# Optimization experiments

Hardware: AMD Instinct MI355X
Metric: run time of the kernel (lower is better)

## Reference

```python
import jax, jax.numpy as jnp
import numpy as np

STD = 0.5
B = 1048576
DIM = 8  # arch == 2
_LOG_STD = -0.6931471805599453       # log(0.5)
_HALF_LOG_2PI = 0.9189385332046727   # 0.5*log(2*pi)


def _mlp(x, w1, b1, w2, b2):
    # Sequential(Linear, ReLU, Linear)
    return jnp.maximum(x @ w1 + b1, 0.0) @ w2 + b2


def _bce_sum(logits, targets):
    # BCEWithLogitsLoss(reduction='sum'), numerically stable
    return jnp.sum(jnp.maximum(logits, 0.0) - logits * targets
                   + jnp.log1p(jnp.exp(-jnp.abs(logits))))


def _normal_logprob_sum(mu, y):
    # D.Normal(mu, STD).log_prob(y).sum()
    return jnp.sum(-0.5 * ((y - mu) / STD) ** 2 - _LOG_STD - _HALF_LOG_2PI)


def setup_inputs() -> dict:
    key = jax.random.key(0)
    keys = iter(jax.random.split(key, 64))

    def nrm(shape, s=1.0):
        return s * jax.random.normal(next(keys), shape, dtype=jnp.float32)

    inp = {
        'y1': nrm((B, 1)),
        'y2': nrm((B, 1)),
        'n1': jax.random.uniform(next(keys), (B, 2), dtype=jnp.float32),
        'n2': jax.random.uniform(next(keys), (B, 2), dtype=jnp.float32),
        'n3': jax.random.uniform(next(keys), (B, 2), dtype=jnp.float32),
        'n4': jax.random.uniform(next(keys), (B, 2), dtype=jnp.float32),
    }
    # (name, d_in, d_out) for every 2-layer MLP in infnet/gennet
    mlp_specs = [('inf0', 2, 2), ('inf1', 3, 2), ('inf2', 1, 2), ('inf3', 2, 2),
                 ('g1', 2, 2), ('g2', 2, 1), ('g3', 1, 2), ('g4', 2, 2), ('g5', 2, 1)]
    for name, din, dout in mlp_specs:
        inp[name + '_w1'] = nrm((din, DIM), 0.5)
        inp[name + '_b1'] = nrm((DIM,), 0.1)
        inp[name + '_w2'] = nrm((DIM, dout), 0.5)
        inp[name + '_b2'] = nrm((dout,), 0.1)
    inp['g0_w'] = nrm((1, 2), 0.5)  # gennet[0]: Linear(1, z, bias=False)
    return inp


def reference(y1, y2, n1, n2, n3, n4,
              inf0_w1, inf0_b1, inf0_w2, inf0_b2,
              inf1_w1, inf1_b1, inf1_w2, inf1_b2,
              inf2_w1, inf2_b1, inf2_w2, inf2_b2,
              inf3_w1, inf3_b1, inf3_w2, inf3_b2,
              g1_w1, g1_b1, g1_w2, g1_b2,
              g2_w1, g2_b1, g2_w2, g2_b2,
              g3_w1, g3_b1, g3_w2, g3_b2,
              g4_w1, g4_b1, g4_w2, g4_b2,
              g5_w1, g5_b1, g5_w2, g5_b2,
              g0_w):
    b = y1.shape[0]
    # ---- infer(): recognition pass with hard Bernoulli samples ----
    pz1 = jax.nn.sigmoid(_mlp(jnp.concatenate([y1, y2], axis=1),
                              inf0_w1, inf0_b1, inf0_w2, inf0_b2))
    z1 = (pz1 > n1).astype(jnp.float32)
    pz2 = jax.nn.sigmoid(_mlp(jnp.concatenate([y2, z1], axis=1),
                              inf1_w1, inf1_b1, inf1_w2, inf1_b2))
    z2 = (pz2 > n2).astype(jnp.float32)
    pz3 = jax.nn.sigmoid(_mlp(y2, inf2_w1, inf2_b1, inf2_w2, inf2_b2))
    z3 = (pz3 > n3).astype(jnp.float32)
    pz4 = jax.nn.sigmoid(_mlp(z3, inf3_w1, inf3_b1, inf3_w2, inf3_b2))
    z4 = (pz4 > n4).astype(jnp.float32)
    # ---- generate_wake(): generative logits conditioned on inferred latents ----
    l4 = jnp.ones((b, 1), jnp.float32) @ g0_w          # [B, 2]
    l3 = _mlp(z4, g1_w1, g1_b1, g1_w2, g1_b2)          # [B, 2]
    muy2 = _mlp(z3, g2_w1, g2_b1, g2_w2, g2_b2)        # [B, 1]
    l2 = _mlp(y2, g3_w1, g3_b1, g3_w2, g3_b2)          # [B, 2]
    l1 = _mlp(z2, g4_w1, g4_b1, g4_w2, g4_b2)          # [B, 2]
    muy1 = _mlp(z1, g5_w1, g5_b1, g5_w2, g5_b2)        # [B, 1]
    # ---- wake losses ----
    bf = jnp.float32(b)
    loss_z = (_bce_sum(l1, z1) + _bce_sum(l2, z2)
              + _bce_sum(l3, z3) + _bce_sum(l4, z4)) / bf
    loss_y = (-_normal_logprob_sum(muy1, y1)
              - _normal_logprob_sum(muy2, y2)) / bf
    return (loss_z + loss_y, loss_z, loss_y)
```

## Files before the change

### kernel.cpp

```cpp
#include <hip/hip_runtime.h>
#include <math.h>

#define NBLK 4096
#define NT 256
#define TBL_OFF (NBLK * 8)

typedef float f32x2 __attribute__((ext_vector_type(2)));

__device__ __forceinline__ f32x2 relu2(f32x2 v) {
    f32x2 z = {0.0f, 0.0f};
    return __builtin_elementwise_max(v, z);
}
__device__ __forceinline__ float zsel(float s, float n) {
    float e = __expf(-s);
    return (1.0f - n > n * e) ? 1.0f : 0.0f;
}
__device__ __forceinline__ float sp_f(float l) {
    return fmaxf(l, 0.0f) + __logf(1.0f + __expf(-fabsf(l)));
}

__global__ __launch_bounds__(64) void make_tables(
    const float* __restrict__ i3w1, const float* __restrict__ i3b1,
    const float* __restrict__ i3w2, const float* __restrict__ i3b2,
    const float* __restrict__ g1w1, const float* __restrict__ g1b1,
    const float* __restrict__ g1w2, const float* __restrict__ g1b2,
    const float* __restrict__ g2w1, const float* __restrict__ g2b1,
    const float* __restrict__ g2w2, const float* __restrict__ g2b2,
    const float* __restrict__ g4w1, const float* __restrict__ g4b1,
    const float* __restrict__ g4w2, const float* __restrict__ g4b2,
    const float* __restrict__ g5w1, const float* __restrict__ g5b1,
    const float* __restrict__ g5w2, const float* __restrict__ g5b2,
    float* __restrict__ tbl)
{
    __shared__ float lds_eval[5][4][2];
    const int tid = threadIdx.x;
    if (tid < 20) {
        const int m = tid >> 2, c = tid & 3;
        const float z0 = (float)(c & 1), z1f = (float)(c >> 1);
        const float *w1, *bb1, *w2, *bb2; int dout;
        switch (m) {
            case 0:  w1 = i3w1; bb1 = i3b1; w2 = i3w2; bb2 = i3b2; dout = 2; break;
            case 1:  w1 = g1w1; bb1 = g1b1; w2 = g1w2; bb2 = g1b2; dout = 2; break;
            case 2:  w1 = g2w1; bb1 = g2b1; w2 = g2w2; bb2 = g2b2; dout = 1; break;
            case 3:  w1 = g4w1; bb1 = g4b1; w2 = g4w2; bb2 = g4b2; dout = 2; break;
            default: w1 = g5w1; bb1 = g5b1; w2 = g5w2; bb2 = g5b2; dout = 1; break;
        }
        float o0 = bb2[0];
        float o1 = (dout == 2) ? bb2[1] : 0.0f;
        #pragma unroll
        for (int j = 0; j < 8; ++j) {
            float h = fmaxf(bb1[j] + z0 * w1[j] + z1f * w1[8 + j], 0.0f);
            o0 += h * w2[j * dout];
            if (dout == 2) o1 += h * w2[j * 2 + 1];
        }
        lds_eval[m][c][0] = o0;
        lds_eval[m][c][1] = o1;
    }
    __syncthreads();
    if (tid < 12) {
        const int pair = tid >> 1, elem = tid & 1;
        int m, k, tf;
        switch (tid) {
            case 0:  m = 0; k = 0; tf = 1; break;
            case 1:  m = 0; k = 1; tf = 1; break;
            case 2:  m = 1; k = 0; tf = 0; break;
            case 3:  m = 1; k = 1; tf = 0; break;
            case 4:  m = 1; k = 0; tf = 2; break;
            case 5:  m = 1; k = 1; tf = 2; break;
            case 6:  m = 3; k = 0; tf = 0; break;
            case 7:  m = 3; k = 1; tf = 0; break;
            case 8:  m = 3; k = 0; tf = 2; break;
            case 9:  m = 3; k = 1; tf = 2; break;
            case 10: m = 2; k = 0; tf = 0; break;
            default: m = 4; k = 0; tf = 0; break;
        }
        float f[4];
        #pragma unroll
        for (int c = 0; c < 4; ++c) {
            float x = lds_eval[m][c][k];
            if (tf == 1)      x = 1.0f / (1.0f + expf(-x));
            else if (tf == 2) x = fmaxf(x, 0.0f) + log1pf(expf(-fabsf(x)));
            f[c] = x;
        }
        tbl[(pair * 4 + 0) * 2 + elem] = f[0];
        tbl[(pair * 4 + 1) * 2 + elem] = f[1] - f[0];
        tbl[(pair * 4 + 2) * 2 + elem] = f[2] - f[0];
        tbl[(pair * 4 + 3) * 2 + elem] = f[3] - f[1] - f[2] + f[0];
    }
}

#define WPAIR(ptr, idx) (f32x2{(ptr)[idx], (ptr)[(idx) + 1]})

__global__ __launch_bounds__(NT, 6) void wake_main(
    const float* __restrict__ y1, const float* __restrict__ y2,
    const float* __restrict__ n1, const float* __restrict__ n2,
    const float* __restrict__ n3, const float* __restrict__ n4,
    const float* __restrict__ i0w1, const float* __restrict__ i0b1,
    const float* __restrict__ i0w2, const float* __restrict__ i0b2,
    const float* __restrict__ i1w1, const float* __restrict__ i1b1,
    const float* __restrict__ i1w2, const float* __restrict__ i1b2,
    const float* __restrict__ i2w1, const float* __restrict__ i2b1,
    const float* __restrict__ i2w2, const float* __restrict__ i2b2,
    const float* __restrict__ g3w1, const float* __restrict__ g3b1,
    const float* __restrict__ g3w2, const float* __restrict__ g3b2,
    const float* __restrict__ g0w,
    const float* __restrict__ tbl,
    float2* __restrict__ partials)
{
    const int tid = threadIdx.x;
    const int g = blockIdx.x * NT + tid;

    const float Y1 = y1[g];
    const float Y2 = y2[g];
    const float2 N1 = reinterpret_cast<const float2*>(n1)[g];
    const float2 N2 = reinterpret_cast<const float2*>(n2)[g];
    const float2 N3 = reinterpret_cast<const float2*>(n3)[g];
    const float2 N4 = reinterpret_cast<const float2*>(n4)[g];

    f32x2 acc0 = WPAIR(i0b2, 0);
    #pragma unroll
    for (int jp = 0; jp < 4; ++jp) {
        const int j = 2 * jp;
        f32x2 h = relu2(WPAIR(i0b1, j) + Y1 * WPAIR(i0w1, j) + Y2 * WPAIR(i0w1, 8 + j));
        acc0 += h.x * WPAIR(i0w2, 2 * j) + h.y * WPAIR(i0w2, 2 * j + 2);
    }
    const float z10 = zsel(acc0.x, N1.x);
    const float z11 = zsel(acc0.y, N1.y);

    f32x2 acc1 = WPAIR(i1b2, 0);
    #pragma unroll
    for (int jp = 0; jp < 4; ++jp) {
        const int j = 2 * jp;
        f32x2 h = relu2(WPAIR(i1b1, j) + Y2 * WPAIR(i1w1, j)
                        + z10 * WPAIR(i1w1, 8 + j) + z11 * WPAIR(i1w1, 16 + j));
        acc1 += h.x * WPAIR(i1w2, 2 * j) + h.y * WPAIR(i1w2, 2 * j + 2);
    }
    const float z20 = zsel(acc1.x, N2.x);
    const float z21 = zsel(acc1.y, N2.y);

    f32x2 acc2 = WPAIR(i2b2, 0);
    #pragma unroll
    for (int jp = 0; jp < 4; ++jp) {
        const int j = 2 * jp;
        f32x2 h = relu2(WPAIR(i2b1, j) + Y2 * WPAIR(i2w1, j));
        acc2 += h.x * WPAIR(i2w2, 2 * j) + h.y * WPAIR(i2w2, 2 * j + 2);
    }
    const float z30 = zsel(acc2.x, N3.x);
    const float z31 = zsel(acc2.y, N3.y);

    const float p3 = z30 * z31;
    const f32x2 sg = WPAIR(tbl, 0) + z30 * WPAIR(tbl, 2) + z31 * WPAIR(tbl, 4) + p3 * WPAIR(tbl, 6);
    const float z40 = (sg.x > N4.x) ? 1.0f : 0.0f;
    const float z41 = (sg.y > N4.y) ? 1.0f : 0.0f;
    const float p4 = z40 * z41;

    f32x2 l2 = WPAIR(g3b2, 0);
    #pragma unroll
    for (int jp = 0; jp < 4; ++jp) {
        const int j = 2 * jp;
        f32x2 h = relu2(WPAIR(g3b1, j) + Y2 * WPAIR(g3w1, j));
        l2 += h.x * WPAIR(g3w2, 2 * j) + h.y * WPAIR(g3w2, 2 * j + 2);
    }

    const f32x2 l3  = WPAIR(tbl, 8)  + z40 * WPAIR(tbl, 10) + z41 * WPAIR(tbl, 12) + p4 * WPAIR(tbl, 14);
    const f32x2 SP3 = WPAIR(tbl, 16) + z40 * WPAIR(tbl, 18) + z41 * WPAIR(tbl, 20) + p4 * WPAIR(tbl, 22);
    const float p2 = z20 * z21;
    const f32x2 l1  = WPAIR(tbl, 24) + z20 * WPAIR(tbl, 26) + z21 * WPAIR(tbl, 28) + p2 * WPAIR(tbl, 30);
    const f32x2 SP1 = WPAIR(tbl, 32) + z20 * WPAIR(tbl, 34) + z21 * WPAIR(tbl, 36) + p2 * WPAIR(tbl, 38);
    const float p1 = z10 * z11;
    const f32x2 zA = {z30, z10}, zB = {z31, z11}, zP = {p3, p1};
    const f32x2 mu = WPAIR(tbl, 40) + zA * WPAIR(tbl, 42) + zB * WPAIR(tbl, 44) + zP * WPAIR(tbl, 46);
    const float L40 = g0w[0], L41 = g0w[1];

    const f32x2 z1v = {z10, z11}, z2v = {z20, z21}, z3v = {z30, z31};
    f32x2 sp2 = {sp_f(l2.x), sp_f(l2.y)};
    f32x2 bsum = (SP1 - l1 * z1v) + (SP3 - l3 * z3v) + (sp2 - l2 * z2v);
    float lz = bsum.x + bsum.y - (L40 * z40 + L41 * z41);
    const f32x2 d = {Y2 - mu.x, Y1 - mu.y};
    const f32x2 dd = d * d;
    float ly = dd.x + dd.y;

    #pragma unroll
    for (int off = 32; off > 0; off >>= 1) {
        lz += __shfl_down(lz, off);
        ly += __shfl_down(ly, off);
    }
    __shared__ float2 wsum[NT / 64];
    const int lane = tid & 63, wid = tid >> 6;
    if (lane == 0) wsum[wid] = make_float2(lz, ly);
    __syncthreads();
    if (tid == 0) {
        float a = 0.0f, b = 0.0f;
        #pragma unroll
        for (int w = 0; w < NT / 64; ++w) { a += wsum[w].x; b += wsum[w].y; }
        partials[blockIdx.x] = make_float2(a, b);
    }
}

__global__ __launch_bounds__(256) void wake_reduce(
    const float2* __restrict__ partials, const float* __restrict__ g0w,
    float* __restrict__ out)
{
    const int tid = threadIdx.x;
    float lz = 0.0f, ly = 0.0f;
    #pragma unroll
    for (int i = 0; i < NBLK / 256; ++i) {
        float2 p = partials[tid + i * 256];
        lz += p.x; ly += p.y;
    }
    #pragma unroll
    for (int off = 32; off > 0; off >>= 1) {
        lz += __shfl_down(lz, off);
        ly += __shfl_down(ly, off);
    }
    __shared__ float2 wsum[4];
    const int lane = tid & 63, wid = tid >> 6;
    if (lane == 0) wsum[wid] = make_float2(lz, ly);
    __syncthreads();
    if (tid == 0) {
        float a = 0.0f, b = 0.0f;
        #pragma unroll
        for (int w = 0; w < 4; ++w) { a += wsum[w].x; b += wsum[w].y; }
        const float l40 = g0w[0], l41 = g0w[1];
        const float c4 = fmaxf(l40, 0.0f) + log1pf(expf(-fabsf(l40)))
                       + fmaxf(l41, 0.0f) + log1pf(expf(-fabsf(l41)));
        const float inv = 1.0f / 1048576.0f;
        const float loss_z = a * inv + c4;
        const float loss_y = 2.0f * b * inv + 0.4515827052894548f;
        out[0] = loss_z + loss_y;
        out[1] = loss_z;
        out[2] = loss_y;
    }
}

extern "C" void kernel_launch(void* const* d_in, const int* in_sizes, int n_in,
                              void* d_out, int out_size, void* d_ws, size_t ws_size,
                              hipStream_t stream) {
    const float* p[43];
    for (int i = 0; i < 43; ++i) p[i] = (const float*)d_in[i];
    float2* partials = (float2*)d_ws;
    float* tbl = (float*)((char*)d_ws + TBL_OFF);

    make_tables<<<1, 64, 0, stream>>>(
        p[18], p[19], p[20], p[21],
        p[22], p[23], p[24], p[25],
        p[26], p[27], p[28], p[29],
        p[34], p[35], p[36], p[37],
        p[38], p[39], p[40], p[41],
        tbl);
    wake_main<<<NBLK, NT, 0, stream>>>(
        p[0], p[1], p[2], p[3], p[4], p[5],
        p[6], p[7], p[8], p[9],
        p[10], p[11], p[12], p[13],
        p[14], p[15], p[16], p[17],
        p[30], p[31], p[32], p[33],
        p[42], tbl, partials);
    wake_reduce<<<1, 256, 0, stream>>>(partials, p[42], (float*)d_out);
}
```

Baseline: 25.17 us.

## Fuse lookup-table construction into main kernel via per-block LDS tables

Removes the separate single-block make_tables launch and has every block of the main kernel recompute the small MLP lookup tables into shared memory, followed by a barrier. This drops one kernel launch and its serial dependency, along with the global-memory round trip for the table. In exchange, each of the 4096 blocks repeats the table math, including transcendentals, in its first 20 threads and adds a __syncthreads before the main compute.

```diff
diff --git a/kernel.cpp b/kernel.cpp
--- a/kernel.cpp
+++ b/kernel.cpp
@@ -3,7 +3,6 @@
 
 #define NBLK 4096
 #define NT 256
-#define TBL_OFF (NBLK * 8)
 
 typedef float f32x2 __attribute__((ext_vector_type(2)));
 
@@ -19,21 +18,46 @@
     return fmaxf(l, 0.0f) + __logf(1.0f + __expf(-fabsf(l)));
 }
 
-__global__ __launch_bounds__(64) void make_tables(
+#define WPAIR(ptr, idx) (f32x2{(ptr)[idx], (ptr)[(idx) + 1]})
+
+__global__ __launch_bounds__(NT, 6) void wake_main(
+    const float* __restrict__ y1, const float* __restrict__ y2,
+    const float* __restrict__ n1, const float* __restrict__ n2,
+    const float* __restrict__ n3, const float* __restrict__ n4,
+    const float* __restrict__ i0w1, const float* __restrict__ i0b1,
+    const float* __restrict__ i0w2, const float* __restrict__ i0b2,
+    const float* __restrict__ i1w1, const float* __restrict__ i1b1,
+    const float* __restrict__ i1w2, const float* __restrict__ i1b2,
+    const float* __restrict__ i2w1, const float* __restrict__ i2b1,
+    const float* __restrict__ i2w2, const float* __restrict__ i2b2,
     const float* __restrict__ i3w1, const float* __restrict__ i3b1,
     const float* __restrict__ i3w2, const float* __restrict__ i3b2,
     const float* __restrict__ g1w1, const float* __restrict__ g1b1,
     const float* __restrict__ g1w2, const float* __restrict__ g1b2,
     const float* __restrict__ g2w1, const float* __restrict__ g2b1,
     const float* __restrict__ g2w2, const float* __restrict__ g2b2,
+    const float* __restrict__ g3w1, const float* __restrict__ g3b1,
+    const float* __restrict__ g3w2, const float* __restrict__ g3b2,
     const float* __restrict__ g4w1, const float* __restrict__ g4b1,
     const float* __restrict__ g4w2, const float* __restrict__ g4b2,
     const float* __restrict__ g5w1, const float* __restrict__ g5b1,
     const float* __restrict__ g5w2, const float* __restrict__ g5b2,
-    float* __restrict__ tbl)
+    const float* __restrict__ g0w,
+    float2* __restrict__ partials)
 {
     __shared__ float lds_eval[5][4][2];
+    __shared__ __align__(8) float lds_coef[48];
+
     const int tid = threadIdx.x;
+    const int g = blockIdx.x * NT + tid;
+
+    const float Y1 = y1[g];
+    const float Y2 = y2[g];
+    const float2 N1 = reinterpret_cast<const float2*>(n1)[g];
+    const float2 N2 = reinterpret_cast<const float2*>(n2)[g];
+    const float2 N3 = reinterpret_cast<const float2*>(n3)[g];
+    const float2 N4 = reinterpret_cast<const float2*>(n4)[g];
+
     if (tid < 20) {
         const int m = tid >> 2, c = tid & 3;
         const float z0 = (float)(c & 1), z1f = (float)(c >> 1);
@@ -82,40 +106,14 @@
             else if (tf == 2) x = fmaxf(x, 0.0f) + log1pf(expf(-fabsf(x)));
             f[c] = x;
         }
-        tbl[(pair * 4 + 0) * 2 + elem] = f[0];
-        tbl[(pair * 4 + 1) * 2 + elem] = f[1] - f[0];
-        tbl[(pair * 4 + 2) * 2 + elem] = f[2] - f[0];
-        tbl[(pair * 4 + 3) * 2 + elem] = f[3] - f[1] - f[2] + f[0];
-    }
-}
-
-#define WPAIR(ptr, idx) (f32x2{(ptr)[idx], (ptr)[(idx) + 1]})
-
-__global__ __launch_bounds__(NT, 6) void wake_main(
-    const float* __restrict__ y1, const float* __restrict__ y2,
-    const float* __restrict__ n1, const float* __restrict__ n2,
-    const float* __restrict__ n3, const float* __restrict__ n4,
-    const float* __restrict__ i0w1, const float* __restrict__ i0b1,
-    const float* __restrict__ i0w2, const float* __restrict__ i0b2,
-    const float* __restrict__ i1w1, const float* __restrict__ i1b1,
-    const float* __restrict__ i1w2, const float* __restrict__ i1b2,
-    const float* __restrict__ i2w1, const float* __restrict__ i2b1,
-    const float* __restrict__ i2w2, const float* __restrict__ i2b2,
-    const float* __restrict__ g3w1, const float* __restrict__ g3b1,
-    const float* __restrict__ g3w2, const float* __restrict__ g3b2,
-    const float* __restrict__ g0w,
-    const float* __restrict__ tbl,
-    float2* __restrict__ partials)
-{
-    const int tid = threadIdx.x;
-    const int g = blockIdx.x * NT + tid;
-
-    const float Y1 = y1[g];
-    const float Y2 = y2[g];
-    const float2 N1 = reinterpret_cast<const float2*>(n1)[g];
-    const float2 N2 = reinterpret_cast<const float2*>(n2)[g];
-    const float2 N3 = reinterpret_cast<const float2*>(n3)[g];
-    const float2 N4 = reinterpret_cast<const float2*>(n4)[g];
+        lds_coef[(pair * 4 + 0) * 2 + elem] = f[0];
+        lds_coef[(pair * 4 + 1) * 2 + elem] = f[1] - f[0];
+        lds_coef[(pair * 4 + 2) * 2 + elem] = f[2] - f[0];
+        lds_coef[(pair * 4 + 3) * 2 + elem] = f[3] - f[1] - f[2] + f[0];
+    }
+    __syncthreads();
+
+    #define LPAIR(idx) (f32x2{lds_coef[idx], lds_coef[(idx) + 1]})
 
     f32x2 acc0 = WPAIR(i0b2, 0);
     #pragma unroll
@@ -149,7 +147,7 @@
     const float z31 = zsel(acc2.y, N3.y);
 
     const float p3 = z30 * z31;
-    const f32x2 sg = WPAIR(tbl, 0) + z30 * WPAIR(tbl, 2) + z31 * WPAIR(tbl, 4) + p3 * WPAIR(tbl, 6);
+    const f32x2 sg = LPAIR(0) + z30 * LPAIR(2) + z31 * LPAIR(4) + p3 * LPAIR(6);
     const float z40 = (sg.x > N4.x) ? 1.0f : 0.0f;
     const float z41 = (sg.y > N4.y) ? 1.0f : 0.0f;
     const float p4 = z40 * z41;
@@ -162,14 +160,14 @@
         l2 += h.x * WPAIR(g3w2, 2 * j) + h.y * WPAIR(g3w2, 2 * j + 2);
     }
 
-    const f32x2 l3  = WPAIR(tbl, 8)  + z40 * WPAIR(tbl, 10) + z41 * WPAIR(tbl, 12) + p4 * WPAIR(tbl, 14);
-    const f32x2 SP3 = WPAIR(tbl, 16) + z40 * WPAIR(tbl, 18) + z41 * WPAIR(tbl, 20) + p4 * WPAIR(tbl, 22);
+    const f32x2 l3  = LPAIR(8)  + z40 * LPAIR(10) + z41 * LPAIR(12) + p4 * LPAIR(14);
+    const f32x2 SP3 = LPAIR(16) + z40 * LPAIR(18) + z41 * LPAIR(20) + p4 * LPAIR(22);
     const float p2 = z20 * z21;
-    const f32x2 l1  = WPAIR(tbl, 24) + z20 * WPAIR(tbl, 26) + z21 * WPAIR(tbl, 28) + p2 * WPAIR(tbl, 30);
-    const f32x2 SP1 = WPAIR(tbl, 32) + z20 * WPAIR(tbl, 34) + z21 * WPAIR(tbl, 36) + p2 * WPAIR(tbl, 38);
+    const f32x2 l1  = LPAIR(24) + z20 * LPAIR(26) + z21 * LPAIR(28) + p2 * LPAIR(30);
+    const f32x2 SP1 = LPAIR(32) + z20 * LPAIR(34) + z21 * LPAIR(36) + p2 * LPAIR(38);
     const float p1 = z10 * z11;
     const f32x2 zA = {z30, z10}, zB = {z31, z11}, zP = {p3, p1};
-    const f32x2 mu = WPAIR(tbl, 40) + zA * WPAIR(tbl, 42) + zB * WPAIR(tbl, 44) + zP * WPAIR(tbl, 46);
+    const f32x2 mu = LPAIR(40) + zA * LPAIR(42) + zB * LPAIR(44) + zP * LPAIR(46);
     const float L40 = g0w[0], L41 = g0w[1];
 
     const f32x2 z1v = {z10, z11}, z2v = {z20, z21}, z3v = {z30, z31};
@@ -239,21 +237,18 @@
     const float* p[43];
     for (int i = 0; i < 43; ++i) p[i] = (const float*)d_in[i];
     float2* partials = (float2*)d_ws;
-    float* tbl = (float*)((char*)d_ws + TBL_OFF);
-
-    make_tables<<<1, 64, 0, stream>>>(
-        p[18], p[19], p[20], p[21],
-        p[22], p[23], p[24], p[25],
-        p[26], p[27], p[28], p[29],
-        p[34], p[35], p[36], p[37],
-        p[38], p[39], p[40], p[41],
-        tbl);
+
     wake_main<<<NBLK, NT, 0, stream>>>(
         p[0], p[1], p[2], p[3], p[4], p[5],
         p[6], p[7], p[8], p[9],
         p[10], p[11], p[12], p[13],
         p[14], p[15], p[16], p[17],
+        p[18], p[19], p[20], p[21],
+        p[22], p[23], p[24], p[25],
+        p[26], p[27], p[28], p[29],
         p[30], p[31], p[32], p[33],
-        p[42], tbl, partials);
+        p[34], p[35], p[36], p[37],
+        p[38], p[39], p[40], p[41],
+        p[42], partials);
     wake_reduce<<<1, 256, 0, stream>>>(partials, p[42], (float*)d_out);
 }
```

Result: slower. 31.52 us (+25.2%).
